# Performance work log

Measured on AMD Instinct MI355X. Metric: run time of the kernel, lower is better.

The kernel has to match this reference:

```python
import jax, jax.numpy as jnp
import numpy as np

B, H, W, C = 8, 64, 64, 512
CK, CV = C // 8, C // 2  # 64, 256


def maxpool2x2(x):
    # x: [B, H, W, C] -> [B, H//2, W//2, C], 2x2 max pool, stride 2 (keras MaxPooling2D default)
    b, h, w, c = x.shape
    return x.reshape(b, h // 2, 2, w // 2, 2, c).max(axis=(2, 4))


def setup_inputs() -> dict:
    key = jax.random.key(0)
    ks = jax.random.split(key, 6)
    wscale = 0.02
    return {
        "x": jax.random.normal(ks[0], (B, H, W, C), dtype=jnp.float32),
        "w_theta": jax.random.normal(ks[1], (C, CK), dtype=jnp.float32) * wscale,
        "w_phi": jax.random.normal(ks[2], (C, CK), dtype=jnp.float32) * wscale,
        "w_g": jax.random.normal(ks[3], (C, CV), dtype=jnp.float32) * wscale,
        "w_o": jax.random.normal(ks[4], (CV, C), dtype=jnp.float32) * wscale,
        "gamma": jax.random.normal(ks[5], (1,), dtype=jnp.float32),
    }


def reference(x, w_theta, w_phi, w_g, w_o, gamma):
    b, h, w, c = x.shape
    hw = h * w
    # theta: 1x1 conv -> [B, HW, C//8]
    theta = jnp.einsum('bhwc,ck->bhwk', x, w_theta).reshape(b, hw, -1)
    # phi: 1x1 conv + 2x2 maxpool -> [B, HW//4, C//8]
    phi = maxpool2x2(jnp.einsum('bhwc,ck->bhwk', x, w_phi)).reshape(b, hw // 4, -1)
    # attention: [B, HW, HW//4], softmax over last axis
    attn = jax.nn.softmax(jnp.einsum('bqk,bpk->bqp', theta, phi), axis=-1)
    # g: 1x1 conv + 2x2 maxpool -> [B, HW//4, C//2]
    g = maxpool2x2(jnp.einsum('bhwc,cv->bhwv', x, w_g)).reshape(b, hw // 4, -1)
    # attn_g: [B, HW, C//2] -> [B, H, W, C//2] -> 1x1 conv -> [B, H, W, C]
    attn_g = jnp.einsum('bqp,bpv->bqv', attn, g).reshape(b, h, w, -1)
    attn_g = jnp.einsum('bhwv,vc->bhwc', attn_g, w_o)
    return x + gamma * attn_g
```

## Files before the change

kernel.cpp:

```cpp
#include <hip/hip_runtime.h>
#include <hip/hip_bf16.h>
#include <cstddef>
#include <cstdint>


typedef __attribute__((ext_vector_type(8))) short short8;
typedef __attribute__((ext_vector_type(4))) float float4v;

namespace {
constexpr int kB = 8, kC = 512, kCK = 64, kCV = 256, kHW = 4096, kP = 1024;
constexpr int kNP = 384;
}

__device__ __forceinline__ void gll16(const void* g, void* l) {
  __builtin_amdgcn_global_load_lds((uint32_t __attribute__((address_space(1)))*)g,
                                   (uint32_t __attribute__((address_space(3)))*)l,
                                   16, 0, 0);
}
__device__ __forceinline__ float4v mfma16(short8 a, short8 b, float4v c) {
  return __builtin_amdgcn_mfma_f32_16x16x32_bf16(a, b, c, 0, 0, 0);
}
__device__ __forceinline__ const short8* fragp(const char* tile, int row, int oct) {
  return (const short8*)(tile + row * 128 + ((oct ^ (row & 7)) * 16));
}

__global__ __launch_bounds__(256) void k_pack_w(
    const float* __restrict__ wt, const float* __restrict__ wphi,
    const float* __restrict__ wg, const float* __restrict__ wo,
    __hip_bfloat16* __restrict__ wAll, __hip_bfloat16* __restrict__ woT) {
  int idx = blockIdx.x * 256 + threadIdx.x;
  if (idx < 196608) {
    int n = idx >> 9, k = idx & 511;
    float v = (n < 64) ? wt[k * 64 + n]
            : (n < 128) ? wphi[k * 64 + (n - 64)]
                        : wg[k * 256 + (n - 128)];
    wAll[idx] = __float2bfloat16(v);
  } else {
    int t = idx - 196608;
    int n = t >> 8, k = t & 255;
    woT[t] = __float2bfloat16(wo[k * 512 + n]);
  }
}

__global__ __launch_bounds__(256) void k_proj(const float* __restrict__ x,
                                              const __hip_bfloat16* __restrict__ wAll,
                                              __hip_bfloat16* __restrict__ pgf) {
  __shared__ __align__(16) char smem[16384 + 49152];
  char* As = smem;
  char* Bs = smem + 16384;
  const int tid = threadIdx.x, wid = tid >> 6, lane = tid & 63;
  const int m = lane & 15, quad = lane >> 4;
  const int row0 = blockIdx.x * 64;
  const int wm = (wid >> 1) * 32, wn = (wid & 1) * 192;
  float4v acc[2][12] = {};
  for (int kc = 0; kc < 512; kc += 64) {
#pragma unroll
    for (int u = 0; u < 4; ++u) {
      const int r0 = (wid * 4 + u) * 4;
      const int row = r0 + (lane >> 4);
      const int sqg = (lane & 15) ^ (row & 15);
      gll16(x + (size_t)(row0 + row) * 512 + kc + sqg * 4, As + r0 * 256);
    }
#pragma unroll
    for (int u = 0; u < 12; ++u) {
      const int r0 = (wid * 12 + u) * 8;
      const int row = r0 + (lane >> 3);
      const int og = (lane & 7) ^ (row & 7);
      gll16(wAll + (size_t)row * 512 + kc + og * 8, Bs + r0 * 128);
    }
    __syncthreads();
#pragma unroll
    for (int kk = 0; kk < 64; kk += 32) {
      short8 af[2];
#pragma unroll
      for (int i = 0; i < 2; ++i) {
        const int row = wm + i * 16 + m;
        const int sq0 = (kk >> 2) + quad * 2;
        float4v lo = *(const float4v*)(As + row * 256 + ((sq0 ^ m) * 16));
        float4v hi = *(const float4v*)(As + row * 256 + (((sq0 + 1) ^ m) * 16));
        short8 a;
        a[0] = __builtin_bit_cast(short, __float2bfloat16(lo[0]));
        a[1] = __builtin_bit_cast(short, __float2bfloat16(lo[1]));
        a[2] = __builtin_bit_cast(short, __float2bfloat16(lo[2]));
        a[3] = __builtin_bit_cast(short, __float2bfloat16(lo[3]));
        a[4] = __builtin_bit_cast(short, __float2bfloat16(hi[0]));
        a[5] = __builtin_bit_cast(short, __float2bfloat16(hi[1]));
        a[6] = __builtin_bit_cast(short, __float2bfloat16(hi[2]));
        a[7] = __builtin_bit_cast(short, __float2bfloat16(hi[3]));
        af[i] = a;
      }
      const int oct = (kk >> 3) + quad;
#pragma unroll
      for (int j = 0; j < 12; ++j) {
        short8 bf = *fragp(Bs, wn + j * 16 + m, oct);
#pragma unroll
        for (int i = 0; i < 2; ++i) acc[i][j] = mfma16(af[i], bf, acc[i][j]);
      }
    }
    __syncthreads();
  }
#pragma unroll
  for (int i = 0; i < 2; ++i)
#pragma unroll
    for (int j = 0; j < 12; ++j)
#pragma unroll
      for (int r = 0; r < 4; ++r)
        pgf[(size_t)(row0 + wm + i * 16 + quad * 4 + r) * 384 + wn + j * 16 + m] =
            __float2bfloat16(acc[i][j][r]);
}

__global__ __launch_bounds__(256) void k_pool_phi(const __hip_bfloat16* __restrict__ pg,
                                                  __hip_bfloat16* __restrict__ phi_p) {
  int idx = blockIdx.x * 256 + threadIdx.x;
  int c = idx & 63;
  int p = (idx >> 6) & 1023;
  int b = idx >> 16;
  int ph = p >> 5, pw = p & 31;
  size_t base = ((size_t)b * 4096 + ph * 128 + pw * 2) * kNP + 64 + c;
  float v0 = __bfloat162float(pg[base]);
  float v1 = __bfloat162float(pg[base + kNP]);
  float v2 = __bfloat162float(pg[base + kNP * 64]);
  float v3 = __bfloat162float(pg[base + kNP * 64 + kNP]);
  phi_p[idx] = __float2bfloat16(fmaxf(fmaxf(v0, v1), fmaxf(v2, v3)));
}

__global__ __launch_bounds__(256) void k_pool_gT(const __hip_bfloat16* __restrict__ pg,
                                                 __hip_bfloat16* __restrict__ gT) {
  __shared__ __hip_bfloat16 t[64][65];
  const int p0 = blockIdx.x * 64, v0 = blockIdx.y * 64, b = blockIdx.z;
#pragma unroll
  for (int it = 0; it < 16; ++it) {
    int li = it * 256 + threadIdx.x;
    int pp = li >> 6, v = li & 63;
    int p = p0 + pp;
    int ph = p >> 5, pw = p & 31;
    size_t base = ((size_t)b * 4096 + ph * 128 + pw * 2) * kNP + 128 + v0 + v;
    float mv = fmaxf(
        fmaxf(__bfloat162float(pg[base]), __bfloat162float(pg[base + kNP])),
        fmaxf(__bfloat162float(pg[base + kNP * 64]), __bfloat162float(pg[base + kNP * 64 + kNP])));
    t[pp][v] = __float2bfloat16(mv);
  }
  __syncthreads();
#pragma unroll
  for (int it = 0; it < 16; ++it) {
    int li = it * 256 + threadIdx.x;
    int v = li >> 6, p = li & 63;
    gT[((size_t)b * 256 + v0 + v) * 1024 + p0 + p] = t[p][v];
  }
}

__global__ __launch_bounds__(512, 4) void k_fattn(
    const __hip_bfloat16* __restrict__ pgf,
    const __hip_bfloat16* __restrict__ phip,
    const __hip_bfloat16* __restrict__ gT,
    __hip_bfloat16* __restrict__ O) {
  __shared__ __align__(16) char smem[65536 + 1024 + 128];
  char* P = smem;
  float* pred = (float*)(smem + 65536);
  float* rowstat = (float*)(smem + 65536 + 1024);

  const int tid = threadIdx.x, wid = tid >> 6, lane = tid & 63;
  const int m = lane & 15, quad = lane >> 4;
  const int bid = blockIdx.x;
  const int b = bid & 7;
  const int q0 = (bid >> 3) * 32;

  short8 aq[2][2];
  const __hip_bfloat16* qb = pgf + (size_t)(b * kHW + q0) * kNP;
#pragma unroll
  for (int i = 0; i < 2; ++i)
#pragma unroll
    for (int t = 0; t < 2; ++t)
      aq[i][t] = *(const short8*)(qb + (size_t)(i * 16 + m) * kNP + t * 32 + quad * 8);

  const __hip_bfloat16* kbp = phip + ((size_t)b * kP + wid * 128) * 64;
  float4v sc[2][8] = {};
  short8 kf[2][2];
#pragma unroll
  for (int t = 0; t < 2; ++t)
    kf[0][t] = *(const short8*)(kbp + (size_t)m * 64 + t * 32 + quad * 8);
#pragma unroll
  for (int c = 0; c < 8; ++c) {
    if (c < 7) {
#pragma unroll
      for (int t = 0; t < 2; ++t)
        kf[(c + 1) & 1][t] =
            *(const short8*)(kbp + (size_t)((c + 1) * 16 + m) * 64 + t * 32 + quad * 8);
    }
#pragma unroll
    for (int t = 0; t < 2; ++t)
#pragma unroll
      for (int i = 0; i < 2; ++i) sc[i][c] = mfma16(aq[i][t], kf[c & 1][t], sc[i][c]);
  }

  float mx[2][4];
#pragma unroll
  for (int i = 0; i < 2; ++i)
#pragma unroll
    for (int r = 0; r < 4; ++r) {
      float v = sc[i][0][r];
#pragma unroll
      for (int s = 1; s < 8; ++s) v = fmaxf(v, sc[i][s][r]);
#pragma unroll
      for (int d = 1; d < 16; d <<= 1) v = fmaxf(v, __shfl_xor(v, d));
      mx[i][r] = v;
    }
  if (m == 0) {
#pragma unroll
    for (int i = 0; i < 2; ++i)
#pragma unroll
      for (int r = 0; r < 4; ++r) pred[(i * 16 + quad * 4 + r) * 8 + wid] = mx[i][r];
  }
  __syncthreads();
  if (tid < 32) {
    float v = pred[tid * 8];
#pragma unroll
    for (int w = 1; w < 8; ++w) v = fmaxf(v, pred[tid * 8 + w]);
    rowstat[tid] = v;
  }
  __syncthreads();
  float sm[2][4];
#pragma unroll
  for (int i = 0; i < 2; ++i)
#pragma unroll
    for (int r = 0; r < 4; ++r) {
      const float rm = rowstat[i * 16 + quad * 4 + r];
      float s = 0.f;
#pragma unroll
      for (int ss = 0; ss < 8; ++ss) {
        float e = __expf(sc[i][ss][r] - rm);
        sc[i][ss][r] = e;
        s += e;
      }
#pragma unroll
      for (int d = 1; d < 16; d <<= 1) s += __shfl_xor(s, d);
      sm[i][r] = s;
    }
  __syncthreads();
  if (m == 0) {
#pragma unroll
    for (int i = 0; i < 2; ++i)
#pragma unroll
      for (int r = 0; r < 4; ++r) pred[(i * 16 + quad * 4 + r) * 8 + wid] = sm[i][r];
  }
  __syncthreads();
  if (tid < 32) {
    float s = 0.f;
#pragma unroll
    for (int w = 0; w < 8; ++w) s += pred[tid * 8 + w];
    rowstat[tid] = 1.f / s;
  }

#pragma unroll
  for (int i = 0; i < 2; ++i)
#pragma unroll
    for (int c = 0; c < 8; ++c)
#pragma unroll
      for (int r = 0; r < 4; ++r) {
        const int row = i * 16 + quad * 4 + r;
        const int key = wid * 128 + c * 16 + m;
        const int oct = (key >> 3) ^ (row & 15);
        *(__hip_bfloat16*)(P + row * 2048 + oct * 16 + (key & 7) * 2) =
            __float2bfloat16(sc[i][c][r]);
      }
  __syncthreads();

  const __hip_bfloat16* gb = gT + ((size_t)b * kCV + wid * 32) * kP;
  float4v oc[2][2] = {};
  short8 gf[2][2], af[2][2];
#pragma unroll
  for (int j = 0; j < 2; ++j)
    gf[0][j] = *(const short8*)(gb + (size_t)(j * 16 + m) * kP + quad * 8);
#pragma unroll
  for (int i = 0; i < 2; ++i) {
    const int row = i * 16 + m;
    af[0][i] = *(const short8*)(P + row * 2048 + ((quad ^ (row & 15)) * 16));
  }
#pragma unroll
  for (int cp = 0; cp < 32; ++cp) {
    const int cur = cp & 1;
    if (cp < 31) {
      const int p0n = (cp + 1) * 32;
#pragma unroll
      for (int j = 0; j < 2; ++j)
        gf[cur ^ 1][j] = *(const short8*)(gb + (size_t)(j * 16 + m) * kP + p0n + quad * 8);
#pragma unroll
      for (int i = 0; i < 2; ++i) {
        const int row = i * 16 + m;
        const int oct = ((cp + 1) * 4 + quad) ^ (row & 15);
        af[cur ^ 1][i] = *(const short8*)(P + row * 2048 + oct * 16);
      }
    }
#pragma unroll
    for (int i = 0; i < 2; ++i)
#pragma unroll
      for (int j = 0; j < 2; ++j) oc[i][j] = mfma16(af[cur][i], gf[cur][j], oc[i][j]);
  }

  const float r0v = rowstat[quad * 4 + 0];
#pragma unroll
  for (int i = 0; i < 2; ++i)
#pragma unroll
    for (int j = 0; j < 2; ++j)
#pragma unroll
      for (int r = 0; r < 4; ++r) {
        const int row = i * 16 + quad * 4 + r;
        O[((size_t)b * kHW + q0 + row) * kCV + wid * 32 + j * 16 + m] =
            __float2bfloat16(oc[i][j][r] * rowstat[row]);
      }
  (void)r0v;
}

__global__ __launch_bounds__(256) void k_out(const __hip_bfloat16* __restrict__ A,
                                             const __hip_bfloat16* __restrict__ Bw,
                                             const float* __restrict__ x,
                                             const float* __restrict__ gamma,
                                             float* __restrict__ out) {
  __shared__ __align__(16) char smem[4 * 16384];
  const int tid = threadIdx.x, wid = tid >> 6, lane = tid & 63;
  const int m = lane & 15, quad = lane >> 4;
  const int row0 = blockIdx.x * 128, col0 = blockIdx.y * 128;
  const int wm = (wid >> 1) * 64, wn = (wid & 1) * 64;
  float4v acc[4][4] = {};
  auto stage = [&](int t, int buf) {
    const int kc = t * 64;
#pragma unroll
    for (int u = 0; u < 4; ++u) {
      const int r0 = (wid * 4 + u) * 8;
      const int row = r0 + (lane >> 3);
      const int og = (lane & 7) ^ (row & 7);
      gll16(A + (size_t)(row0 + row) * 256 + kc + og * 8, smem + buf * 16384 + r0 * 128);
      gll16(Bw + (size_t)(col0 + row) * 256 + kc + og * 8,
            smem + 32768 + buf * 16384 + r0 * 128);
    }
  };
  stage(0, 0);
  __syncthreads();
#pragma unroll
  for (int t = 0; t < 4; ++t) {
    if (t < 3) stage(t + 1, (t + 1) & 1);
    const char* Ab = smem + (t & 1) * 16384;
    const char* Bb = smem + 32768 + (t & 1) * 16384;
    __builtin_amdgcn_s_setprio(1);
#pragma unroll
    for (int kk = 0; kk < 64; kk += 32) {
      const int oct = (kk >> 3) + quad;
      short8 af[4], bf[4];
#pragma unroll
      for (int i = 0; i < 4; ++i) af[i] = *fragp(Ab, wm + i * 16 + m, oct);
#pragma unroll
      for (int j = 0; j < 4; ++j) bf[j] = *fragp(Bb, wn + j * 16 + m, oct);
#pragma unroll
      for (int i = 0; i < 4; ++i)
#pragma unroll
        for (int j = 0; j < 4; ++j) acc[i][j] = mfma16(af[i], bf[j], acc[i][j]);
    }
    __builtin_amdgcn_s_setprio(0);
    __syncthreads();
  }
  const float g = gamma[0];
#pragma unroll
  for (int i = 0; i < 4; ++i)
#pragma unroll
    for (int j = 0; j < 4; ++j) {
      const int cc = col0 + wn + j * 16 + m;
      const int rb = row0 + wm + i * 16 + quad * 4;
#pragma unroll
      for (int r = 0; r < 4; ++r) {
        const size_t idx = (size_t)(rb + r) * 512 + cc;
        out[idx] = x[idx] + g * acc[i][j][r];
      }
    }
}

extern "C" void kernel_launch(void* const* d_in, const int* in_sizes, int n_in,
                              void* d_out, int out_size, void* d_ws, size_t ws_size,
                              hipStream_t stream) {
  (void)in_sizes; (void)n_in; (void)out_size; (void)ws_size;
  const float* x     = (const float*)d_in[0];
  const float* wt    = (const float*)d_in[1];
  const float* wphi  = (const float*)d_in[2];
  const float* wg    = (const float*)d_in[3];
  const float* wo    = (const float*)d_in[4];
  const float* gamma = (const float*)d_in[5];
  float* out = (float*)d_out;

  char* ws = (char*)d_ws;
  __hip_bfloat16* wAll = (__hip_bfloat16*)(ws);
  __hip_bfloat16* woT  = (__hip_bfloat16*)(ws + 393216);
  __hip_bfloat16* pgf  = (__hip_bfloat16*)(ws + 655360);
  __hip_bfloat16* phip = (__hip_bfloat16*)(ws + 25821184);
  __hip_bfloat16* gT   = (__hip_bfloat16*)(ws + 26869760);
  __hip_bfloat16* O    = (__hip_bfloat16*)(ws + 31064064);

  k_pack_w<<<1280, 256, 0, stream>>>(wt, wphi, wg, wo, wAll, woT);
  k_proj<<<512, 256, 0, stream>>>(x, wAll, pgf);
  k_pool_phi<<<2048, 256, 0, stream>>>(pgf, phip);
  k_pool_gT<<<dim3(16, 4, 8), 256, 0, stream>>>(pgf, gT);
  k_fattn<<<dim3(kHW / 32 * kB), 512, 0, stream>>>(pgf, phip, gT, O);
  k_out<<<dim3(256, 4), 256, 0, stream>>>(O, woT, x, gamma, out);
}
```

Before: 256.6 us.

## Process 64 query rows per attention block with 16 waves to reuse gT loads

The fused attention kernel now handles 64 query rows per block with 1024 threads. Score computation is split across two query halves and eight key slices. The PV stage assigns each wave 16 value columns across all 64 rows, so each gT fragment feeds four MFMAs instead of being loaded separately per 32-row block. This halves global traffic on gT, at the cost of 130KB+ LDS per block (one block per CU), no LDS prefetch of the P fragments, and a different swizzle and barrier layout.

```diff
diff --git a/kernel.cpp b/kernel.cpp
--- a/kernel.cpp
+++ b/kernel.cpp
@@ -149,31 +149,33 @@
   }
 }
 
-__global__ __launch_bounds__(512, 4) void k_fattn(
+__global__ __launch_bounds__(1024) void k_fattn(
     const __hip_bfloat16* __restrict__ pgf,
     const __hip_bfloat16* __restrict__ phip,
     const __hip_bfloat16* __restrict__ gT,
     __hip_bfloat16* __restrict__ O) {
-  __shared__ __align__(16) char smem[65536 + 1024 + 128];
+  __shared__ __align__(16) char smem[131072 + 2048 + 256];
   char* P = smem;
-  float* pred = (float*)(smem + 65536);
-  float* rowstat = (float*)(smem + 65536 + 1024);
+  float* pred = (float*)(smem + 131072);
+  float* rowstat = (float*)(smem + 131072 + 2048);
 
   const int tid = threadIdx.x, wid = tid >> 6, lane = tid & 63;
   const int m = lane & 15, quad = lane >> 4;
   const int bid = blockIdx.x;
   const int b = bid & 7;
-  const int q0 = (bid >> 3) * 32;
+  const int q0 = (bid >> 3) * 64;
+  const int qh = wid & 1;
+  const int kw = wid >> 1;
 
   short8 aq[2][2];
-  const __hip_bfloat16* qb = pgf + (size_t)(b * kHW + q0) * kNP;
+  const __hip_bfloat16* qb = pgf + (size_t)(b * kHW + q0 + qh * 32) * kNP;
 #pragma unroll
   for (int i = 0; i < 2; ++i)
 #pragma unroll
     for (int t = 0; t < 2; ++t)
       aq[i][t] = *(const short8*)(qb + (size_t)(i * 16 + m) * kNP + t * 32 + quad * 8);
 
-  const __hip_bfloat16* kbp = phip + ((size_t)b * kP + wid * 128) * 64;
+  const __hip_bfloat16* kbp = phip + ((size_t)b * kP + kw * 128) * 64;
   float4v sc[2][8] = {};
   short8 kf[2][2];
 #pragma unroll
@@ -209,10 +211,11 @@
 #pragma unroll
     for (int i = 0; i < 2; ++i)
 #pragma unroll
-      for (int r = 0; r < 4; ++r) pred[(i * 16 + quad * 4 + r) * 8 + wid] = mx[i][r];
-  }
-  __syncthreads();
-  if (tid < 32) {
+      for (int r = 0; r < 4; ++r)
+        pred[(qh * 32 + i * 16 + quad * 4 + r) * 8 + kw] = mx[i][r];
+  }
+  __syncthreads();
+  if (tid < 64) {
     float v = pred[tid * 8];
 #pragma unroll
     for (int w = 1; w < 8; ++w) v = fmaxf(v, pred[tid * 8 + w]);
@@ -224,7 +227,7 @@
   for (int i = 0; i < 2; ++i)
 #pragma unroll
     for (int r = 0; r < 4; ++r) {
-      const float rm = rowstat[i * 16 + quad * 4 + r];
+      const float rm = rowstat[qh * 32 + i * 16 + quad * 4 + r];
       float s = 0.f;
 #pragma unroll
       for (int ss = 0; ss < 8; ++ss) {
@@ -236,20 +239,21 @@
       for (int d = 1; d < 16; d <<= 1) s += __shfl_xor(s, d);
       sm[i][r] = s;
     }
-  __syncthreads();
   if (m == 0) {
 #pragma unroll
     for (int i = 0; i < 2; ++i)
 #pragma unroll
-      for (int r = 0; r < 4; ++r) pred[(i * 16 + quad * 4 + r) * 8 + wid] = sm[i][r];
-  }
-  __syncthreads();
-  if (tid < 32) {
+      for (int r = 0; r < 4; ++r)
+        pred[(qh * 32 + i * 16 + quad * 4 + r) * 8 + kw] = sm[i][r];
+  }
+  __syncthreads();
+  if (tid < 64) {
     float s = 0.f;
 #pragma unroll
     for (int w = 0; w < 8; ++w) s += pred[tid * 8 + w];
     rowstat[tid] = 1.f / s;
   }
+  __syncthreads();
 
 #pragma unroll
   for (int i = 0; i < 2; ++i)
@@ -257,58 +261,43 @@
     for (int c = 0; c < 8; ++c)
 #pragma unroll
       for (int r = 0; r < 4; ++r) {
-        const int row = i * 16 + quad * 4 + r;
-        const int key = wid * 128 + c * 16 + m;
-        const int oct = (key >> 3) ^ (row & 15);
-        *(__hip_bfloat16*)(P + row * 2048 + oct * 16 + (key & 7) * 2) =
+        const int row = qh * 32 + i * 16 + quad * 4 + r;
+        const int key = kw * 128 + c * 16 + m;
+        const int oct = key >> 3;
+        const int oc2 = (oct & 0x70) | ((oct & 15) ^ (row & 15));
+        *(__hip_bfloat16*)(P + row * 2048 + oc2 * 16 + (key & 7) * 2) =
             __float2bfloat16(sc[i][c][r]);
       }
   __syncthreads();
 
-  const __hip_bfloat16* gb = gT + ((size_t)b * kCV + wid * 32) * kP;
-  float4v oc[2][2] = {};
-  short8 gf[2][2], af[2][2];
-#pragma unroll
-  for (int j = 0; j < 2; ++j)
-    gf[0][j] = *(const short8*)(gb + (size_t)(j * 16 + m) * kP + quad * 8);
-#pragma unroll
-  for (int i = 0; i < 2; ++i) {
-    const int row = i * 16 + m;
-    af[0][i] = *(const short8*)(P + row * 2048 + ((quad ^ (row & 15)) * 16));
-  }
+  const __hip_bfloat16* gbase = gT + ((size_t)b * kCV + wid * 16 + m) * kP;
+  float4v oc[4] = {};
+  short8 gf[2];
+  gf[0] = *(const short8*)(gbase + quad * 8);
 #pragma unroll
   for (int cp = 0; cp < 32; ++cp) {
     const int cur = cp & 1;
-    if (cp < 31) {
-      const int p0n = (cp + 1) * 32;
-#pragma unroll
-      for (int j = 0; j < 2; ++j)
-        gf[cur ^ 1][j] = *(const short8*)(gb + (size_t)(j * 16 + m) * kP + p0n + quad * 8);
-#pragma unroll
-      for (int i = 0; i < 2; ++i) {
-        const int row = i * 16 + m;
-        const int oct = ((cp + 1) * 4 + quad) ^ (row & 15);
-        af[cur ^ 1][i] = *(const short8*)(P + row * 2048 + oct * 16);
-      }
-    }
-#pragma unroll
-    for (int i = 0; i < 2; ++i)
-#pragma unroll
-      for (int j = 0; j < 2; ++j) oc[i][j] = mfma16(af[cur][i], gf[cur][j], oc[i][j]);
-  }
-
-  const float r0v = rowstat[quad * 4 + 0];
-#pragma unroll
-  for (int i = 0; i < 2; ++i)
-#pragma unroll
-    for (int j = 0; j < 2; ++j)
-#pragma unroll
-      for (int r = 0; r < 4; ++r) {
-        const int row = i * 16 + quad * 4 + r;
-        O[((size_t)b * kHW + q0 + row) * kCV + wid * 32 + j * 16 + m] =
-            __float2bfloat16(oc[i][j][r] * rowstat[row]);
-      }
-  (void)r0v;
+    if (cp < 31) gf[cur ^ 1] = *(const short8*)(gbase + (cp + 1) * 32 + quad * 8);
+    short8 af[4];
+#pragma unroll
+    for (int i = 0; i < 4; ++i) {
+      const int row = i * 16 + m;
+      const int oct = cp * 4 + quad;
+      const int oc2 = (oct & 0x70) | ((oct & 15) ^ (row & 15));
+      af[i] = *(const short8*)(P + row * 2048 + oc2 * 16);
+    }
+#pragma unroll
+    for (int i = 0; i < 4; ++i) oc[i] = mfma16(af[i], gf[cur], oc[i]);
+  }
+
+#pragma unroll
+  for (int i = 0; i < 4; ++i)
+#pragma unroll
+    for (int r = 0; r < 4; ++r) {
+      const int row = i * 16 + quad * 4 + r;
+      O[((size_t)b * kHW + q0 + row) * kCV + wid * 16 + m] =
+          __float2bfloat16(oc[i][r] * rowstat[row]);
+    }
 }
 
 __global__ __launch_bounds__(256) void k_out(const __hip_bfloat16* __restrict__ A,
@@ -397,6 +386,6 @@
   k_proj<<<512, 256, 0, stream>>>(x, wAll, pgf);
   k_pool_phi<<<2048, 256, 0, stream>>>(pgf, phip);
   k_pool_gT<<<dim3(16, 4, 8), 256, 0, stream>>>(pgf, gT);
-  k_fattn<<<dim3(kHW / 32 * kB), 512, 0, stream>>>(pgf, phip, gT, O);
+  k_fattn<<<dim3(kHW / 64 * kB), 1024, 0, stream>>>(pgf, phip, gT, O);
   k_out<<<dim3(256, 4), 256, 0, stream>>>(O, woT, x, gamma, out);
 }
```

Result: faster. 234.9 us (-8.5%).
